# Performance work log

Measured on AMD Instinct MI355X. Metric: run time of the kernel, lower is better.

Reference implementation:

```python
import jax, jax.numpy as jnp
import numpy as np

EMBED = 1024
HEADS = 16
HEAD_DIM = EMBED // HEADS


def setup_inputs() -> dict:
    key = jax.random.key(0)
    ks = jax.random.split(key, 8)
    B, S = 2, 2048
    inp = {
        "values": jax.random.normal(ks[0], (B, S, EMBED), jnp.float32),
        "keys": jax.random.normal(ks[1], (B, S, EMBED), jnp.float32),
        "queries": jax.random.normal(ks[2], (B, S, EMBED), jnp.float32),
        # per-head projection weights (torch Linear: y = x @ W.T), shared across heads
        "Wv": jax.random.normal(ks[3], (HEAD_DIM, HEAD_DIM), jnp.float32) / np.sqrt(HEAD_DIM),
        "Wk": jax.random.normal(ks[4], (HEAD_DIM, HEAD_DIM), jnp.float32) / np.sqrt(HEAD_DIM),
        "Wq": jax.random.normal(ks[5], (HEAD_DIM, HEAD_DIM), jnp.float32) / np.sqrt(HEAD_DIM),
        "Wo": jax.random.normal(ks[6], (EMBED, EMBED), jnp.float32) / np.sqrt(EMBED),
        "bo": jax.random.normal(ks[7], (EMBED,), jnp.float32) * 0.02,
    }
    return inp


def reference(values, keys, queries, Wv, Wk, Wq, Wo, bo):
    B, S, _ = queries.shape
    # split heads: (B, H, S, D)
    def split(x):
        return x.reshape(B, -1, HEADS, HEAD_DIM).transpose(0, 2, 1, 3)
    v, k, q = split(values), split(keys), split(queries)
    # per-head linear projections (no bias): x @ W.T
    v = jnp.einsum('bhsd,ed->bhse', v, Wv)
    k = jnp.einsum('bhsd,ed->bhse', k, Wk)
    q = jnp.einsum('bhsd,ed->bhse', q, Wq)
    # scaled dot-product attention (naive, full matrix)
    scores = jnp.einsum('bhqd,bhkd->bhqk', q, k) / jnp.sqrt(jnp.float32(HEAD_DIM))
    attn = jax.nn.softmax(scores, axis=-1)
    out = jnp.einsum('bhqk,bhkd->bhqd', attn, v)
    # merge heads and output projection
    out = out.transpose(0, 2, 1, 3).reshape(B, S, EMBED)
    return out @ Wo.T + bo
```

## Files before the change

kernel.cpp:

```cpp
#include <hip/hip_runtime.h>
#include <stdint.h>

#define HEADS 16
#define HD    64
#define SEQ   2048
#define BATCH 2
#define EMB   1024

using short8  = __attribute__((ext_vector_type(8))) short;
using float4v = __attribute__((ext_vector_type(4))) float;

__device__ __forceinline__ unsigned int f2bfr(float f) {
    return (__float_as_uint(f) + 0x8000u) >> 16;
}

__device__ __forceinline__ unsigned int dpp_xor1(unsigned int x) {
    return (unsigned int)__builtin_amdgcn_update_dpp(0, (int)x, 0xB1, 0xF, 0xF, true);
}

__global__ __launch_bounds__(256) void cvt_wo_kernel(const float* __restrict__ Wo,
                                                     unsigned short* __restrict__ Wob) {
    int i = (blockIdx.x * 256 + threadIdx.x) * 4;
    float4 v = *(const float4*)(Wo + i);
    uint2 o;
    o.x = f2bfr(v.x) | (f2bfr(v.y) << 16);
    o.y = f2bfr(v.z) | (f2bfr(v.w) << 16);
    *(uint2*)(Wob + i) = o;
}

__global__ __launch_bounds__(256) void proj_kernel(
    const float* __restrict__ Vx, const float* __restrict__ Kx, const float* __restrict__ Qx,
    const float* __restrict__ Wv, const float* __restrict__ Wk, const float* __restrict__ Wq,
    unsigned short* __restrict__ Qp, unsigned short* __restrict__ Kp,
    unsigned short* __restrict__ Vt) {
    __shared__ __align__(16) unsigned short Ws[64 * 72];
    __shared__ __align__(16) unsigned short xs[64 * 72];
    __shared__ __align__(16) unsigned short vt2[64 * 72];

    const int t = threadIdx.x, w = t >> 6, lane = t & 63, cl = lane & 15, quad = lane >> 4;
    const int z  = blockIdx.z;
    const int bh = blockIdx.y;
    const int b  = bh >> 4, h = bh & 15;
    const int s0 = blockIdx.x * 64;

    const float* x = (z == 0) ? Qx : (z == 1) ? Kx : Vx;
    const float* W = (z == 0) ? Wq : (z == 1) ? Wk : Wv;
    const float scale = (z == 0) ? 0.18033688011112044f : 1.0f;

#pragma unroll
    for (int rep = 0; rep < 4; ++rep) {
        int idx = rep * 1024 + t * 4;
        int e = idx >> 6, d0 = idx & 63;
        float4 w4 = *(const float4*)(W + idx);
        uint2 pk;
        pk.x = f2bfr(w4.x * scale) | (f2bfr(w4.y * scale) << 16);
        pk.y = f2bfr(w4.z * scale) | (f2bfr(w4.w * scale) << 16);
        *(uint2*)(&Ws[e * 72 + d0]) = pk;

        int s = e;
        float4 v4 = *(const float4*)(x + (size_t)(b * SEQ + s0 + s) * EMB + h * 64 + d0);
        uint2 px;
        px.x = f2bfr(v4.x) | (f2bfr(v4.y) << 16);
        px.y = f2bfr(v4.z) | (f2bfr(v4.w) << 16);
        *(uint2*)(&xs[s * 72 + d0]) = px;
    }
    __syncthreads();

    short8 a0 = *(const short8*)(&xs[(w * 16 + cl) * 72 + quad * 8]);
    short8 a1 = *(const short8*)(&xs[(w * 16 + cl) * 72 + 32 + quad * 8]);
    float4v c[4];
#pragma unroll
    for (int nt = 0; nt < 4; ++nt) c[nt] = (float4v){0.f, 0.f, 0.f, 0.f};
#pragma unroll
    for (int nt = 0; nt < 4; ++nt) {
        short8 b0 = *(const short8*)(&Ws[(nt * 16 + cl) * 72 + quad * 8]);
        c[nt] = __builtin_amdgcn_mfma_f32_16x16x32_bf16(a0, b0, c[nt], 0, 0, 0);
        short8 b1 = *(const short8*)(&Ws[(nt * 16 + cl) * 72 + 32 + quad * 8]);
        c[nt] = __builtin_amdgcn_mfma_f32_16x16x32_bf16(a1, b1, c[nt], 0, 0, 0);
    }

    if (z < 2) {
#pragma unroll
        for (int nt = 0; nt < 4; ++nt)
#pragma unroll
            for (int r = 0; r < 4; ++r)
                xs[(w * 16 + quad * 4 + r) * 72 + nt * 16 + cl] =
                    (unsigned short)f2bfr(c[nt][r]);
        unsigned short* outp = (z == 0) ? Qp : Kp;
        int sl = w * 16 + (lane >> 2), c0 = (lane & 3) * 16;
        uint4 o0 = *(const uint4*)(&xs[sl * 72 + c0]);
        uint4 o1 = *(const uint4*)(&xs[sl * 72 + c0 + 8]);
        size_t base = ((size_t)bh * SEQ + s0 + sl) * 64 + c0;
        *(uint4*)(outp + base)     = o0;
        *(uint4*)(outp + base + 8) = o1;
    } else {
#pragma unroll
        for (int nt = 0; nt < 4; ++nt)
#pragma unroll
            for (int r = 0; r < 4; ++r)
                vt2[(nt * 16 + cl) * 72 + w * 16 + quad * 4 + r] =
                    (unsigned short)f2bfr(c[nt][r]);
        __syncthreads();
        int e = t >> 2, sc0 = (t & 3) * 16;
        uint4 o0 = *(const uint4*)(&vt2[e * 72 + sc0]);
        uint4 o1 = *(const uint4*)(&vt2[e * 72 + sc0 + 8]);
        size_t base = ((size_t)bh * 64 + e) * SEQ + s0 + sc0;
        *(uint4*)(Vt + base)     = o0;
        *(uint4*)(Vt + base + 8) = o1;
    }
}

__global__ __launch_bounds__(256) void attn_kernel(
    const unsigned short* __restrict__ Qp, const unsigned short* __restrict__ Kp,
    const unsigned short* __restrict__ Vt, unsigned short* __restrict__ AO) {
    __shared__ __align__(16) unsigned short Ks[2][64 * 72];
    __shared__ __align__(16) unsigned short Vs[2][64 * 72];
    __shared__ __align__(16) unsigned short Ps[4][32 * 72];

    const int t = threadIdx.x;
    const int w = t >> 6, lane = t & 63, cl = lane & 15, quad = lane >> 4;
    const int bh = blockIdx.y;
    const int q0 = blockIdx.x * 128;
    const size_t hbase = (size_t)bh * SEQ * 64;
    const unsigned short* Kbase = Kp + hbase;
    const unsigned short* Vbase = Vt + hbase;

    short8 aq[2][2];
#pragma unroll
    for (int qt = 0; qt < 2; ++qt) {
        size_t rbase = hbase + (size_t)(q0 + w * 32 + qt * 16 + cl) * 64 + quad * 8;
        aq[qt][0] = *(const short8*)(Qp + rbase);
        aq[qt][1] = *(const short8*)(Qp + rbase + 32);
    }

    short8 ones;
#pragma unroll
    for (int i = 0; i < 8; ++i) ones[i] = (short)0x3F80;

    float4v acc[2][5];
#pragma unroll
    for (int qt = 0; qt < 2; ++qt)
#pragma unroll
        for (int nt = 0; nt < 5; ++nt) acc[qt][nt] = (float4v){0.f, 0.f, 0.f, 0.f};

    const int srow = t >> 3;
    const int scol = (t & 7) * 8;

    uint4 kreg[2], vreg[2];
#pragma unroll
    for (int p = 0; p < 2; ++p) {
        int row = srow + p * 32;
        kreg[p] = *(const uint4*)(Kbase + row * 64 + scol);
        vreg[p] = *(const uint4*)(Vbase + (size_t)row * SEQ + scol);
    }

    const int even = ((lane & 1) == 0);
    const unsigned int psel = even ? 0x03020706u : 0x07060302u;
    const int evoff = even ? 0 : 16;
    unsigned int* Pw = (unsigned int*)Ps[w];

    for (int kc = 0; kc < SEQ / 64; ++kc) {
        const int buf = kc & 1;
#pragma unroll
        for (int p = 0; p < 2; ++p) {
            int row = srow + p * 32;
            *(uint4*)(&Ks[buf][row * 72 + scol]) = kreg[p];
            *(uint4*)(&Vs[buf][row * 72 + scol]) = vreg[p];
        }
        __syncthreads();
        if (kc + 1 < SEQ / 64) {
#pragma unroll
            for (int p = 0; p < 2; ++p) {
                int row = srow + p * 32;
                kreg[p] = *(const uint4*)(Kbase + (size_t)(kc + 1) * 4096 + row * 64 + scol);
                vreg[p] = *(const uint4*)(Vbase + (size_t)row * SEQ + (kc + 1) * 64 + scol);
            }
        }

        float4v c[2][4];
#pragma unroll
        for (int qt = 0; qt < 2; ++qt)
#pragma unroll
            for (int nt = 0; nt < 4; ++nt) c[qt][nt] = (float4v){0.f, 0.f, 0.f, 0.f};
#pragma unroll
        for (int nt = 0; nt < 4; ++nt) {
            short8 bk0 = *(const short8*)(&Ks[buf][(nt * 16 + cl) * 72 + quad * 8]);
            short8 bk1 = *(const short8*)(&Ks[buf][(nt * 16 + cl) * 72 + 32 + quad * 8]);
            c[0][nt] = __builtin_amdgcn_mfma_f32_16x16x32_bf16(aq[0][0], bk0, c[0][nt], 0, 0, 0);
            c[0][nt] = __builtin_amdgcn_mfma_f32_16x16x32_bf16(aq[0][1], bk1, c[0][nt], 0, 0, 0);
            c[1][nt] = __builtin_amdgcn_mfma_f32_16x16x32_bf16(aq[1][0], bk0, c[1][nt], 0, 0, 0);
            c[1][nt] = __builtin_amdgcn_mfma_f32_16x16x32_bf16(aq[1][1], bk1, c[1][nt], 0, 0, 0);
        }

#pragma unroll
        for (int qt = 0; qt < 2; ++qt) {
#pragma unroll
            for (int r = 0; r < 4; ++r) {
                unsigned int rr[4], wd[4];
#pragma unroll
                for (int nt = 0; nt < 4; ++nt)
                    rr[nt] = __float_as_uint(__builtin_amdgcn_exp2f(c[qt][nt][r])) + 0x8000u;
#pragma unroll
                for (int nt = 0; nt < 4; ++nt) {
                    unsigned int nb = dpp_xor1(rr[nt]);
                    wd[nt] = __builtin_amdgcn_perm(rr[nt], nb, psel);
                }
                unsigned int wa = even ? wd[0] : wd[2];
                unsigned int wb = even ? wd[1] : wd[3];
                int dwbase = (qt * 16 + quad * 4 + r) * 36 + evoff + (cl >> 1);
                Pw[dwbase]     = wa;
                Pw[dwbase + 8] = wb;
            }
        }

#pragma unroll
        for (int s2i = 0; s2i < 2; ++s2i) {
            short8 ap0 = *(const short8*)(&Ps[w][cl * 72 + s2i * 32 + quad * 8]);
            short8 ap1 = *(const short8*)(&Ps[w][(16 + cl) * 72 + s2i * 32 + quad * 8]);
#pragma unroll
            for (int nt = 0; nt < 4; ++nt) {
                short8 bv = *(const short8*)(&Vs[buf][(nt * 16 + cl) * 72 + s2i * 32 + quad * 8]);
                acc[0][nt] = __builtin_amdgcn_mfma_f32_16x16x32_bf16(ap0, bv, acc[0][nt], 0, 0, 0);
                acc[1][nt] = __builtin_amdgcn_mfma_f32_16x16x32_bf16(ap1, bv, acc[1][nt], 0, 0, 0);
            }
            acc[0][4] = __builtin_amdgcn_mfma_f32_16x16x32_bf16(ap0, ones, acc[0][4], 0, 0, 0);
            acc[1][4] = __builtin_amdgcn_mfma_f32_16x16x32_bf16(ap1, ones, acc[1][4], 0, 0, 0);
        }
    }

#pragma unroll
    for (int qt = 0; qt < 2; ++qt) {
        float inv[4];
#pragma unroll
        for (int r = 0; r < 4; ++r) inv[r] = 1.0f / acc[qt][4][r];
#pragma unroll
        for (int nt = 0; nt < 4; ++nt) {
#pragma unroll
            for (int r = 0; r < 4; ++r) {
                int row = q0 + w * 32 + qt * 16 + quad * 4 + r;
                AO[hbase + (size_t)row * 64 + nt * 16 + cl] =
                    (unsigned short)f2bfr(acc[qt][nt][r] * inv[r]);
            }
        }
    }
}

__global__ __launch_bounds__(256) void outproj_kernel(
    const unsigned short* __restrict__ AO, const unsigned short* __restrict__ Wob,
    const float* __restrict__ bo, float* __restrict__ out) {
    __shared__ __align__(16) unsigned short As[2][64 * 72];
    __shared__ __align__(16) unsigned short Bs[2][64 * 72];

    const int t = threadIdx.x, w = t >> 6, lane = t & 63, cl = lane & 15, quad = lane >> 4;
    const int e0 = blockIdx.x * 64;
    const int m0 = blockIdx.y * 64;
    const int srow = t >> 3, scol = (t & 7) * 8;

    float4v c[4];
#pragma unroll
    for (int nt = 0; nt < 4; ++nt) c[nt] = (float4v){0.f, 0.f, 0.f, 0.f};

    uint4 areg[2], breg[2];
#pragma unroll
    for (int p = 0; p < 2; ++p) {
        int i = srow + p * 32;
        int r = m0 + i, b = r >> 11, s = r & 2047;
        areg[p] = *(const uint4*)(AO + ((size_t)(b * 16 + 0) * SEQ + s) * 64 + scol);
        breg[p] = *(const uint4*)(Wob + (size_t)(e0 + i) * EMB + scol);
    }

    for (int hc = 0; hc < 16; ++hc) {
        const int buf = hc & 1;
#pragma unroll
        for (int p = 0; p < 2; ++p) {
            int i = srow + p * 32;
            *(uint4*)(&As[buf][i * 72 + scol]) = areg[p];
            *(uint4*)(&Bs[buf][i * 72 + scol]) = breg[p];
        }
        __syncthreads();
        if (hc + 1 < 16) {
#pragma unroll
            for (int p = 0; p < 2; ++p) {
                int i = srow + p * 32;
                int r = m0 + i, b = r >> 11, s = r & 2047;
                areg[p] = *(const uint4*)(AO + ((size_t)(b * 16 + hc + 1) * SEQ + s) * 64 + scol);
                breg[p] = *(const uint4*)(Wob + (size_t)(e0 + i) * EMB + (hc + 1) * 64 + scol);
            }
        }
#pragma unroll
        for (int s2i = 0; s2i < 2; ++s2i) {
            short8 a = *(const short8*)(&As[buf][(w * 16 + cl) * 72 + s2i * 32 + quad * 8]);
#pragma unroll
            for (int nt = 0; nt < 4; ++nt) {
                short8 bb = *(const short8*)(&Bs[buf][(nt * 16 + cl) * 72 + s2i * 32 + quad * 8]);
                c[nt] = __builtin_amdgcn_mfma_f32_16x16x32_bf16(a, bb, c[nt], 0, 0, 0);
            }
        }
    }

#pragma unroll
    for (int nt = 0; nt < 4; ++nt) {
        float bias = bo[e0 + nt * 16 + cl];
#pragma unroll
        for (int r = 0; r < 4; ++r) {
            int row = m0 + w * 16 + quad * 4 + r;
            out[(size_t)row * EMB + e0 + nt * 16 + cl] = c[nt][r] + bias;
        }
    }
}

extern "C" void kernel_launch(void* const* d_in, const int* in_sizes, int n_in,
                              void* d_out, int out_size, void* d_ws, size_t ws_size,
                              hipStream_t stream) {
    const float* values  = (const float*)d_in[0];
    const float* keys    = (const float*)d_in[1];
    const float* queries = (const float*)d_in[2];
    const float* Wv = (const float*)d_in[3];
    const float* Wk = (const float*)d_in[4];
    const float* Wq = (const float*)d_in[5];
    const float* Wo = (const float*)d_in[6];
    const float* bo = (const float*)d_in[7];
    float* out = (float*)d_out;

    char* ws = (char*)d_ws;
    unsigned short* Qp  = (unsigned short*)(ws);
    unsigned short* Kp  = (unsigned short*)(ws + (8u  << 20));
    unsigned short* Vt  = (unsigned short*)(ws + (16u << 20));
    unsigned short* AO  = (unsigned short*)(ws + (24u << 20));
    unsigned short* Wob = (unsigned short*)(ws + (32u << 20));

    cvt_wo_kernel<<<dim3(1024), dim3(256), 0, stream>>>(Wo, Wob);
    proj_kernel<<<dim3(SEQ / 64, BATCH * HEADS, 3), dim3(256), 0, stream>>>(
        values, keys, queries, Wv, Wk, Wq, Qp, Kp, Vt);
    attn_kernel<<<dim3(SEQ / 128, BATCH * HEADS), dim3(256), 0, stream>>>(Qp, Kp, Vt, AO);
    outproj_kernel<<<dim3(EMB / 64, (BATCH * SEQ) / 64), dim3(256), 0, stream>>>(
        AO, Wob, bo, out);
}
```

Baseline: 261.5 us.

## Use 32x32 MFMA with transposed scores to keep P in registers

Rewrites the attention inner loop around 32x32x16 bf16 MFMAs, computing K·Q^T so the exponentiated scores land in a layout that becomes the PV A-operand after packed bf16 conversion and a cross-half shuffle. This removes the per-warp LDS staging buffer for P, the DPP/perm packing, and the LDS round trip. It also adds s_setprio around the MFMA blocks and remaps a 1D grid so consecutive blocks spread across heads. The trade-off is higher register pressure from the 16-wide accumulators, plus inline asm for v_cvt_pk_bf16_f32.

```diff
diff --git a/kernel.cpp b/kernel.cpp
--- a/kernel.cpp
+++ b/kernel.cpp
@@ -9,13 +9,23 @@
 
 using short8  = __attribute__((ext_vector_type(8))) short;
 using float4v = __attribute__((ext_vector_type(4))) float;
+using f32x16  = __attribute__((ext_vector_type(16))) float;
 
 __device__ __forceinline__ unsigned int f2bfr(float f) {
     return (__float_as_uint(f) + 0x8000u) >> 16;
 }
 
-__device__ __forceinline__ unsigned int dpp_xor1(unsigned int x) {
-    return (unsigned int)__builtin_amdgcn_update_dpp(0, (int)x, 0xB1, 0xF, 0xF, true);
+__device__ __forceinline__ unsigned int cvt_pk_bf16(float lo, float hi) {
+    unsigned int r;
+    asm("v_cvt_pk_bf16_f32 %0, %1, %2" : "=v"(r) : "v"(lo), "v"(hi));
+    return r;
+}
+
+__device__ __forceinline__ short8 mk8(unsigned int a, unsigned int b,
+                                      unsigned int c, unsigned int d) {
+    union { unsigned int u[4]; short8 s; } x;
+    x.u[0] = a; x.u[1] = b; x.u[2] = c; x.u[3] = d;
+    return x.s;
 }
 
 __global__ __launch_bounds__(256) void cvt_wo_kernel(const float* __restrict__ Wo,
@@ -115,33 +125,33 @@
     const unsigned short* __restrict__ Vt, unsigned short* __restrict__ AO) {
     __shared__ __align__(16) unsigned short Ks[2][64 * 72];
     __shared__ __align__(16) unsigned short Vs[2][64 * 72];
-    __shared__ __align__(16) unsigned short Ps[4][32 * 72];
 
     const int t = threadIdx.x;
-    const int w = t >> 6, lane = t & 63, cl = lane & 15, quad = lane >> 4;
-    const int bh = blockIdx.y;
-    const int q0 = blockIdx.x * 128;
+    const int w = t >> 6, lane = t & 63;
+    const int l31 = lane & 31, h = lane >> 5;
+
+    const int lid = blockIdx.x;
+    const int bh  = ((lid & 7) << 2) | ((lid >> 3) & 3);
+    const int q0  = (lid >> 5) * 128;
+
     const size_t hbase = (size_t)bh * SEQ * 64;
     const unsigned short* Kbase = Kp + hbase;
     const unsigned short* Vbase = Vt + hbase;
 
-    short8 aq[2][2];
-#pragma unroll
-    for (int qt = 0; qt < 2; ++qt) {
-        size_t rbase = hbase + (size_t)(q0 + w * 32 + qt * 16 + cl) * 64 + quad * 8;
-        aq[qt][0] = *(const short8*)(Qp + rbase);
-        aq[qt][1] = *(const short8*)(Qp + rbase + 32);
+    short8 qf[4];
+    {
+        const unsigned short* qr = Qp + hbase + (size_t)(q0 + w * 32 + l31) * 64 + h * 8;
+#pragma unroll
+        for (int dt = 0; dt < 4; ++dt) qf[dt] = *(const short8*)(qr + dt * 16);
     }
 
     short8 ones;
 #pragma unroll
     for (int i = 0; i < 8; ++i) ones[i] = (short)0x3F80;
 
-    float4v acc[2][5];
-#pragma unroll
-    for (int qt = 0; qt < 2; ++qt)
-#pragma unroll
-        for (int nt = 0; nt < 5; ++nt) acc[qt][nt] = (float4v){0.f, 0.f, 0.f, 0.f};
+    f32x16 o0, o1, ls;
+#pragma unroll
+    for (int r = 0; r < 16; ++r) { o0[r] = 0.f; o1[r] = 0.f; ls[r] = 0.f; }
 
     const int srow = t >> 3;
     const int scol = (t & 7) * 8;
@@ -153,11 +163,6 @@
         kreg[p] = *(const uint4*)(Kbase + row * 64 + scol);
         vreg[p] = *(const uint4*)(Vbase + (size_t)row * SEQ + scol);
     }
-
-    const int even = ((lane & 1) == 0);
-    const unsigned int psel = even ? 0x03020706u : 0x07060302u;
-    const int evoff = even ? 0 : 16;
-    unsigned int* Pw = (unsigned int*)Ps[w];
 
     for (int kc = 0; kc < SEQ / 64; ++kc) {
         const int buf = kc & 1;
@@ -177,71 +182,73 @@
             }
         }
 
-        float4v c[2][4];
-#pragma unroll
-        for (int qt = 0; qt < 2; ++qt)
-#pragma unroll
-            for (int nt = 0; nt < 4; ++nt) c[qt][nt] = (float4v){0.f, 0.f, 0.f, 0.f};
-#pragma unroll
-        for (int nt = 0; nt < 4; ++nt) {
-            short8 bk0 = *(const short8*)(&Ks[buf][(nt * 16 + cl) * 72 + quad * 8]);
-            short8 bk1 = *(const short8*)(&Ks[buf][(nt * 16 + cl) * 72 + 32 + quad * 8]);
-            c[0][nt] = __builtin_amdgcn_mfma_f32_16x16x32_bf16(aq[0][0], bk0, c[0][nt], 0, 0, 0);
-            c[0][nt] = __builtin_amdgcn_mfma_f32_16x16x32_bf16(aq[0][1], bk1, c[0][nt], 0, 0, 0);
-            c[1][nt] = __builtin_amdgcn_mfma_f32_16x16x32_bf16(aq[1][0], bk0, c[1][nt], 0, 0, 0);
-            c[1][nt] = __builtin_amdgcn_mfma_f32_16x16x32_bf16(aq[1][1], bk1, c[1][nt], 0, 0, 0);
-        }
-
-#pragma unroll
-        for (int qt = 0; qt < 2; ++qt) {
-#pragma unroll
-            for (int r = 0; r < 4; ++r) {
-                unsigned int rr[4], wd[4];
-#pragma unroll
-                for (int nt = 0; nt < 4; ++nt)
-                    rr[nt] = __float_as_uint(__builtin_amdgcn_exp2f(c[qt][nt][r])) + 0x8000u;
-#pragma unroll
-                for (int nt = 0; nt < 4; ++nt) {
-                    unsigned int nb = dpp_xor1(rr[nt]);
-                    wd[nt] = __builtin_amdgcn_perm(rr[nt], nb, psel);
-                }
-                unsigned int wa = even ? wd[0] : wd[2];
-                unsigned int wb = even ? wd[1] : wd[3];
-                int dwbase = (qt * 16 + quad * 4 + r) * 36 + evoff + (cl >> 1);
-                Pw[dwbase]     = wa;
-                Pw[dwbase + 8] = wb;
-            }
-        }
-
-#pragma unroll
-        for (int s2i = 0; s2i < 2; ++s2i) {
-            short8 ap0 = *(const short8*)(&Ps[w][cl * 72 + s2i * 32 + quad * 8]);
-            short8 ap1 = *(const short8*)(&Ps[w][(16 + cl) * 72 + s2i * 32 + quad * 8]);
-#pragma unroll
-            for (int nt = 0; nt < 4; ++nt) {
-                short8 bv = *(const short8*)(&Vs[buf][(nt * 16 + cl) * 72 + s2i * 32 + quad * 8]);
-                acc[0][nt] = __builtin_amdgcn_mfma_f32_16x16x32_bf16(ap0, bv, acc[0][nt], 0, 0, 0);
-                acc[1][nt] = __builtin_amdgcn_mfma_f32_16x16x32_bf16(ap1, bv, acc[1][nt], 0, 0, 0);
-            }
-            acc[0][4] = __builtin_amdgcn_mfma_f32_16x16x32_bf16(ap0, ones, acc[0][4], 0, 0, 0);
-            acc[1][4] = __builtin_amdgcn_mfma_f32_16x16x32_bf16(ap1, ones, acc[1][4], 0, 0, 0);
-        }
-    }
-
-#pragma unroll
-    for (int qt = 0; qt < 2; ++qt) {
-        float inv[4];
-#pragma unroll
-        for (int r = 0; r < 4; ++r) inv[r] = 1.0f / acc[qt][4][r];
-#pragma unroll
-        for (int nt = 0; nt < 4; ++nt) {
-#pragma unroll
-            for (int r = 0; r < 4; ++r) {
-                int row = q0 + w * 32 + qt * 16 + quad * 4 + r;
-                AO[hbase + (size_t)row * 64 + nt * 16 + cl] =
-                    (unsigned short)f2bfr(acc[qt][nt][r] * inv[r]);
-            }
-        }
+        f32x16 s0, s1;
+#pragma unroll
+        for (int r = 0; r < 16; ++r) { s0[r] = 0.f; s1[r] = 0.f; }
+
+        __builtin_amdgcn_s_setprio(1);
+#pragma unroll
+        for (int dt = 0; dt < 4; ++dt) {
+            short8 k0 = *(const short8*)(&Ks[buf][l31 * 72 + dt * 16 + h * 8]);
+            short8 k1 = *(const short8*)(&Ks[buf][(32 + l31) * 72 + dt * 16 + h * 8]);
+            s0 = __builtin_amdgcn_mfma_f32_32x32x16_bf16(k0, qf[dt], s0, 0, 0, 0);
+            s1 = __builtin_amdgcn_mfma_f32_32x32x16_bf16(k1, qf[dt], s1, 0, 0, 0);
+        }
+        __builtin_amdgcn_s_setprio(0);
+
+#pragma unroll
+        for (int r = 0; r < 16; ++r) {
+            s0[r] = __builtin_amdgcn_exp2f(s0[r]);
+            s1[r] = __builtin_amdgcn_exp2f(s1[r]);
+        }
+
+        short8 fr[4];
+        {
+            unsigned e0 = cvt_pk_bf16(s0[0],  s0[1]),  e1 = cvt_pk_bf16(s0[2],  s0[3]);
+            unsigned e2 = cvt_pk_bf16(s0[4],  s0[5]),  e3 = cvt_pk_bf16(s0[6],  s0[7]);
+            unsigned e4 = cvt_pk_bf16(s0[8],  s0[9]),  e5 = cvt_pk_bf16(s0[10], s0[11]);
+            unsigned e6 = cvt_pk_bf16(s0[12], s0[13]), e7 = cvt_pk_bf16(s0[14], s0[15]);
+            unsigned x0 = __shfl_xor(e0, 32), x1 = __shfl_xor(e1, 32);
+            unsigned x2 = __shfl_xor(e2, 32), x3 = __shfl_xor(e3, 32);
+            unsigned x4 = __shfl_xor(e4, 32), x5 = __shfl_xor(e5, 32);
+            unsigned x6 = __shfl_xor(e6, 32), x7 = __shfl_xor(e7, 32);
+            fr[0] = mk8(h ? x2 : e0, h ? x3 : e1, h ? e2 : x0, h ? e3 : x1);
+            fr[1] = mk8(h ? x6 : e4, h ? x7 : e5, h ? e6 : x4, h ? e7 : x5);
+        }
+        {
+            unsigned e0 = cvt_pk_bf16(s1[0],  s1[1]),  e1 = cvt_pk_bf16(s1[2],  s1[3]);
+            unsigned e2 = cvt_pk_bf16(s1[4],  s1[5]),  e3 = cvt_pk_bf16(s1[6],  s1[7]);
+            unsigned e4 = cvt_pk_bf16(s1[8],  s1[9]),  e5 = cvt_pk_bf16(s1[10], s1[11]);
+            unsigned e6 = cvt_pk_bf16(s1[12], s1[13]), e7 = cvt_pk_bf16(s1[14], s1[15]);
+            unsigned x0 = __shfl_xor(e0, 32), x1 = __shfl_xor(e1, 32);
+            unsigned x2 = __shfl_xor(e2, 32), x3 = __shfl_xor(e3, 32);
+            unsigned x4 = __shfl_xor(e4, 32), x5 = __shfl_xor(e5, 32);
+            unsigned x6 = __shfl_xor(e6, 32), x7 = __shfl_xor(e7, 32);
+            fr[2] = mk8(h ? x2 : e0, h ? x3 : e1, h ? e2 : x0, h ? e3 : x1);
+            fr[3] = mk8(h ? x6 : e4, h ? x7 : e5, h ? e6 : x4, h ? e7 : x5);
+        }
+
+        __builtin_amdgcn_s_setprio(1);
+#pragma unroll
+        for (int c = 0; c < 4; ++c) {
+            short8 bv0 = *(const short8*)(&Vs[buf][l31 * 72 + c * 16 + h * 8]);
+            short8 bv1 = *(const short8*)(&Vs[buf][(32 + l31) * 72 + c * 16 + h * 8]);
+            o0 = __builtin_amdgcn_mfma_f32_32x32x16_bf16(fr[c], bv0, o0, 0, 0, 0);
+            o1 = __builtin_amdgcn_mfma_f32_32x32x16_bf16(fr[c], bv1, o1, 0, 0, 0);
+            ls = __builtin_amdgcn_mfma_f32_32x32x16_bf16(fr[c], ones, ls, 0, 0, 0);
+        }
+        __builtin_amdgcn_s_setprio(0);
+    }
+
+    float inv[16];
+#pragma unroll
+    for (int r = 0; r < 16; ++r) inv[r] = 1.0f / ls[r];
+#pragma unroll
+    for (int r = 0; r < 16; ++r) {
+        int row = q0 + w * 32 + (r & 3) + 8 * (r >> 2) + 4 * h;
+        size_t rb = hbase + (size_t)row * 64 + l31;
+        AO[rb]      = (unsigned short)f2bfr(o0[r] * inv[r]);
+        AO[rb + 32] = (unsigned short)f2bfr(o1[r] * inv[r]);
     }
 }
 
@@ -332,7 +339,7 @@
     cvt_wo_kernel<<<dim3(1024), dim3(256), 0, stream>>>(Wo, Wob);
     proj_kernel<<<dim3(SEQ / 64, BATCH * HEADS, 3), dim3(256), 0, stream>>>(
         values, keys, queries, Wv, Wk, Wq, Qp, Kp, Vt);
-    attn_kernel<<<dim3(SEQ / 128, BATCH * HEADS), dim3(256), 0, stream>>>(Qp, Kp, Vt, AO);
+    attn_kernel<<<dim3((SEQ / 128) * BATCH * HEADS), dim3(256), 0, stream>>>(Qp, Kp, Vt, AO);
     outproj_kernel<<<dim3(EMB / 64, (BATCH * SEQ) / 64), dim3(256), 0, stream>>>(
         AO, Wob, bo, out);
 }
```

After: 258.0 us. No clear change (-1.3%).
